# Optimization experiments

Measured on AMD Instinct MI355X. Metric: run time of the kernel, lower is better.

## Reference

```python
import jax, jax.numpy as jnp
import numpy as np

N = 4096
IN_DIM = 256
HID = 64
NHEADS = 4
OUT_DIM = 128
ALPHA = 0.5  # LeakyReLU negative slope
NEG_INF = -9e15


def gat_layer(x, mask, W, a, concat):
    """Dense GraphAttentionLayer (pyGAT style).
    x:[N,Fin], mask:[N,N] bool, W:[Fin,Fout], a:[2*Fout]."""
    Wh = x @ W                                   # [N, Fout]
    Fout = W.shape[1]
    f1 = Wh @ a[:Fout]                           # [N]
    f2 = Wh @ a[Fout:]                           # [N]
    e = jax.nn.leaky_relu(f1[:, None] + f2[None, :], negative_slope=ALPHA)  # [N,N]
    att = jax.nn.softmax(jnp.where(mask, e, NEG_INF), axis=1)               # [N,N]
    h = att @ Wh                                 # [N, Fout]
    return jax.nn.elu(h) if concat else h


def setup_inputs() -> dict:
    key = jax.random.key(0)
    ks = jax.random.split(key, 6)
    x = jax.random.normal(ks[0], (N, IN_DIM), dtype=jnp.float32)
    adj = jax.random.randint(ks[1], (N, N), 0, 2, dtype=jnp.int32)
    s_in = 1.0 / np.sqrt(IN_DIM)
    s_hid = 1.0 / np.sqrt(HID * NHEADS)
    W_heads = jax.random.uniform(ks[2], (NHEADS, IN_DIM, HID), jnp.float32, -s_in, s_in)
    a_heads = jax.random.uniform(ks[3], (NHEADS, 2 * HID), jnp.float32, -s_in, s_in)
    W_out = jax.random.uniform(ks[4], (HID * NHEADS, OUT_DIM), jnp.float32, -s_hid, s_hid)
    a_out = jax.random.uniform(ks[5], (2 * OUT_DIM,), jnp.float32, -s_hid, s_hid)
    return {"x": x, "adj": adj, "W_heads": W_heads, "a_heads": a_heads,
            "W_out": W_out, "a_out": a_out}


def reference(x, adj, W_heads, a_heads, W_out, a_out):
    mask = adj > 0
    # multi-head attention, concat along feature dim
    heads = jax.vmap(lambda W, a: gat_layer(x, mask, W, a, True))(W_heads, a_heads)
    h = jnp.transpose(heads, (1, 0, 2)).reshape(N, NHEADS * HID)  # [N, H*HID]
    # dropout=0 -> identity; final GAT layer (concat=False) + outer ELU
    out = jax.nn.elu(gat_layer(h, mask, W_out, a_out, False))     # [N, OUT_DIM]
    return out
```

## Files before the change

### kernel.cpp

```cpp
#include <hip/hip_runtime.h>
#include <hip/hip_bf16.h>

#define N 4096
#define IN_DIM 256
#define HID 64
#define NHEADS 4
#define OUT_DIM 128
#define LOG2E 1.44269504088896340736f

typedef __attribute__((ext_vector_type(8))) short bf16x8;
typedef __attribute__((ext_vector_type(4))) float f32x4;

__device__ __forceinline__ ushort2 bsplit(float v) {
    const ushort h = __hip_bfloat16_raw(__float2bfloat16(v)).x;
    const float vh = __uint_as_float((unsigned)h << 16);
    const ushort l = __hip_bfloat16_raw(__float2bfloat16(v - vh)).x;
    return make_ushort2(h, l);
}

__global__ __launch_bounds__(256, 4) void prep_kernel(
        const float* __restrict__ x, const float* __restrict__ W,
        const float* __restrict__ a, const int* __restrict__ adj,
        __hip_bfloat16* __restrict__ WhB,
        float* __restrict__ f1, float* __restrict__ f2,
        unsigned* __restrict__ maskT) {
    const int t = threadIdx.x;
    if (blockIdx.x < 256) {
        const int h = t >> 6, lane = t & 63, m = lane & 15, quad = lane >> 4;
        const int i0 = blockIdx.x * 16;
        const float* xrow = x + (size_t)(i0 + m) * IN_DIM;
        const float* Wp = W + (size_t)h * IN_DIM * HID;
        const f32x4 zero = {0.f, 0.f, 0.f, 0.f};
        f32x4 acc[4] = {zero, zero, zero, zero};
        for (int ks = 0; ks < 8; ks++) {
            const int kb = ks * 32 + quad * 8;
            const float4 xa = *(const float4*)(xrow + kb);
            const float4 xb = *(const float4*)(xrow + kb + 4);
            const float xf[8] = {xa.x, xa.y, xa.z, xa.w, xb.x, xb.y, xb.z, xb.w};
            bf16x8 xh, xl;
#pragma unroll
            for (int e = 0; e < 8; e++) {
                const ushort2 s = bsplit(xf[e]);
                xh[e] = (short)s.x; xl[e] = (short)s.y;
            }
#pragma unroll
            for (int ct = 0; ct < 4; ct++) {
                bf16x8 wh, wl;
#pragma unroll
                for (int e = 0; e < 8; e++) {
                    const ushort2 s =
                        bsplit(Wp[(size_t)(kb + e) * HID + ct * 16 + m]);
                    wh[e] = (short)s.x; wl[e] = (short)s.y;
                }
                acc[ct] = __builtin_amdgcn_mfma_f32_16x16x32_bf16(
                    xh, wh, acc[ct], 0, 0, 0);
                acc[ct] = __builtin_amdgcn_mfma_f32_16x16x32_bf16(
                    xl, wh, acc[ct], 0, 0, 0);
                acc[ct] = __builtin_amdgcn_mfma_f32_16x16x32_bf16(
                    xh, wl, acc[ct], 0, 0, 0);
            }
        }
        const int jblk = i0 >> 5, jb2 = (i0 >> 4) & 1;
#pragma unroll
        for (int ct = 0; ct < 4; ct++) {
#pragma unroll
            for (int r = 0; r < 4; r++) {
                const int jo = quad * 4 + r;
                const int lane_idx = m + 16 * (2 * jb2 + (jo >> 3));
                WhB[((((size_t)h * (N / 32) + jblk) * 4 + ct) * 64 + lane_idx) *
                        8 + (jo & 7)] = __float2bfloat16(acc[ct][r]);
            }
        }
        float av1[4], av2[4];
#pragma unroll
        for (int ct = 0; ct < 4; ct++) {
            av1[ct] = a[h * 2 * HID + ct * 16 + m];
            av2[ct] = a[h * 2 * HID + HID + ct * 16 + m];
        }
        float s1[4], s2[4];
#pragma unroll
        for (int r = 0; r < 4; r++) {
            s1[r] = 0.f; s2[r] = 0.f;
#pragma unroll
            for (int ct = 0; ct < 4; ct++) {
                s1[r] += acc[ct][r] * av1[ct];
                s2[r] += acc[ct][r] * av2[ct];
            }
        }
#pragma unroll
        for (int mm = 8; mm > 0; mm >>= 1) {
#pragma unroll
            for (int r = 0; r < 4; r++) {
                s1[r] += __shfl_xor(s1[r], mm, 64);
                s2[r] += __shfl_xor(s2[r], mm, 64);
            }
        }
        if (m == 0) {
#pragma unroll
            for (int r = 0; r < 4; r++) {
                f1[(size_t)h * N + i0 + quad * 4 + r] = s1[r] * LOG2E;
                f2[(size_t)h * N + i0 + quad * 4 + r] = s2[r] * LOG2E;
            }
        }
    } else {
        const int lane = t & 63, w = t >> 6;
        const int i = (blockIdx.x - 256) * 4 + w;
        const int4* arow = (const int4*)(adj + (size_t)i * N);
        for (int jb = 0; jb < N / 256; jb++) {
            const int4 a4 = arow[jb * 64 + lane];
            unsigned long long bal[4];
            bal[0] = __ballot(a4.x > 0);
            bal[1] = __ballot(a4.y > 0);
            bal[2] = __ballot(a4.z > 0);
            bal[3] = __ballot(a4.w > 0);
            if (lane < 8) {
                unsigned word = 0;
#pragma unroll
                for (int e = 0; e < 4; e++) {
                    unsigned xv = (unsigned)(bal[e] >> (8 * lane)) & 0xFFu;
                    xv = (xv | (xv << 12)) & 0x000F000Fu;
                    xv = (xv | (xv << 6))  & 0x03030303u;
                    xv = (xv | (xv << 3))  & 0x11111111u;
                    word |= xv << e;
                }
                maskT[(size_t)(jb * 8 + lane) * N + i] = word;
            }
        }
    }
}

template <int HEADS, int D, int DSL, int G, int MW>
__global__ __launch_bounds__(G * 64, 4) void attn_fused(
        const unsigned* __restrict__ maskT,
        const __hip_bfloat16* __restrict__ WhB,
        const float* __restrict__ f1g, const float* __restrict__ f2g,
        float* __restrict__ outp) {
    constexpr int CTtot = D / 16;
    constexpr int CTT = CTtot / DSL;
    constexpr int CC = (D == 64) ? 1 : 2;
    constexpr int KSTEPS = N / (32 * G);
    __shared__ float sh[MW * G * 16 * CC * 17];
    __shared__ float dsh[MW * G * 16];
    const int t = threadIdx.x;
    const int g = t >> 6, lane = t & 63;
    const int m = lane & 15, quad = lane >> 4;
    const int h = blockIdx.y / DSL, slc = blockIdx.y % DSL;
    const int i0 = blockIdx.x * (16 * MW);

    float f1v[MW];
#pragma unroll
    for (int mw = 0; mw < MW; mw++)
        f1v[mw] = f1g[(size_t)h * N + i0 + mw * 16 + m];
    const float* f2p = f2g + (size_t)h * N;
    const bf16x8* whb = (const bf16x8*)WhB + (size_t)h * (N / 32) * CTtot * 64;

    const f32x4 zero = {0.f, 0.f, 0.f, 0.f};
    f32x4 acc[MW][CTT];
    f32x4 sac[MW];
#pragma unroll
    for (int mw = 0; mw < MW; mw++) {
        sac[mw] = zero;
#pragma unroll
        for (int ct = 0; ct < CTT; ct++) acc[mw][ct] = zero;
    }
    const short one_bf = (short)0x3F80;
    const bf16x8 ones = {one_bf, one_bf, one_bf, one_bf,
                         one_bf, one_bf, one_bf, one_bf};

    unsigned mwrd[2][MW];
    float f2v[2][8];
    auto stage_mf = [&](int ks, int b) {
        const int j0 = g * (N / G) + ks * 32;
        const int jw = j0 >> 5;
#pragma unroll
        for (int mw = 0; mw < MW; mw++)
            mwrd[b][mw] = maskT[(size_t)jw * N + i0 + mw * 16 + m];
        const float4 lo = *(const float4*)(f2p + j0 + quad * 8);
        const float4 hi = *(const float4*)(f2p + j0 + quad * 8 + 4);
        f2v[b][0] = lo.x; f2v[b][1] = lo.y; f2v[b][2] = lo.z; f2v[b][3] = lo.w;
        f2v[b][4] = hi.x; f2v[b][5] = hi.y; f2v[b][6] = hi.z; f2v[b][7] = hi.w;
    };

    stage_mf(0, 0);
#pragma unroll 2
    for (int ks = 0; ks < KSTEPS; ks++) {
        const int cur = ks & 1;
        const int jwc = (g * (N / G) + ks * 32) >> 5;
        const bf16x8* bp = whb + ((size_t)jwc * CTtot + slc * CTT) * 64 + lane;
        bf16x8 bfrag[CTT];
#pragma unroll
        for (int ct = 0; ct < CTT; ct++) bfrag[ct] = bp[ct * 64];
        if (ks + 1 < KSTEPS) stage_mf(ks + 1, cur ^ 1);
        bf16x8 afr[MW];
#pragma unroll
        for (int mw = 0; mw < MW; mw++) {
            const unsigned mword = mwrd[cur][mw] >> (quad * 8);
            float p[8];
#pragma unroll
            for (int e = 0; e < 8; e++) {
                const float tt = f1v[mw] + f2v[cur][e];
                const float lr = fmaxf(tt, 0.5f * tt);
                const float pe = __builtin_amdgcn_exp2f(lr);
                p[e] = ((mword >> e) & 1u) ? pe : 0.f;
            }
            union { bf16x8 v; __hip_bfloat162 h2[4]; } u;
#pragma unroll
            for (int e2 = 0; e2 < 4; e2++)
                u.h2[e2] = __float22bfloat162_rn(
                    make_float2(p[2 * e2], p[2 * e2 + 1]));
            afr[mw] = u.v;
        }
#pragma unroll
        for (int ct = 0; ct < CTT; ct++)
#pragma unroll
            for (int mw = 0; mw < MW; mw++)
                acc[mw][ct] = __builtin_amdgcn_mfma_f32_16x16x32_bf16(
                    afr[mw], bfrag[ct], acc[mw][ct], 0, 0, 0);
#pragma unroll
        for (int mw = 0; mw < MW; mw++)
            sac[mw] = __builtin_amdgcn_mfma_f32_16x16x32_bf16(
                afr[mw], ones, sac[mw], 0, 0, 0);
    }

#pragma unroll
    for (int rd = 0; rd < CTT / CC; rd++) {
#pragma unroll
        for (int mw = 0; mw < MW; mw++) {
#pragma unroll
            for (int cc = 0; cc < CC; cc++) {
#pragma unroll
                for (int r = 0; r < 4; r++)
                    sh[(((mw * G + g) * 16 + quad * 4 + r) * CC + cc) * 17 + m] =
                        acc[mw][rd * CC + cc][r];
            }
            if (rd == 0 && m == 0) {
#pragma unroll
                for (int r = 0; r < 4; r++)
                    dsh[(mw * G + g) * 16 + quad * 4 + r] = sac[mw][r];
            }
        }
        __syncthreads();
        if (t < 16 * CC * 16) {
            int row, chl;
            if (D == 64) { row = t & 15; chl = (t >> 4) & 15; }
            else         { chl = t & 31; row = (t >> 5) & 15; }
#pragma unroll
            for (int mw = 0; mw < MW; mw++) {
                float av = 0.f, ss = 0.f;
#pragma unroll
                for (int gg = 0; gg < G; gg++) {
                    av += sh[(((mw * G + gg) * 16 + row) * CC + (chl >> 4)) * 17 +
                             (chl & 15)];
                    ss += dsh[(mw * G + gg) * 16 + row];
                }
                float v = av / ss;
                v = (v > 0.f) ? v : (__builtin_amdgcn_exp2f(v * LOG2E) - 1.f);
                const int chg = h * D + slc * (CTT * 16) + rd * CC * 16 + chl;
                const int irow = i0 + mw * 16 + row;
                if (D == 64)
                    outp[(size_t)irow * (NHEADS * HID) + chg] = v;
                else
                    outp[(size_t)irow * D + chg] = v;
            }
        }
        __syncthreads();
    }
}

__global__ __launch_bounds__(512, 2) void gemm2_kernel(
        const float* __restrict__ h1, const float* __restrict__ W2,
        const float* __restrict__ a2, __hip_bfloat16* __restrict__ WhB2,
        float* __restrict__ f1, float* __restrict__ f2) {
    __shared__ float fred[8][16][2];
    const int t = threadIdx.x;
    const int w = t >> 6, lane = t & 63, m = lane & 15, quad = lane >> 4;
    const int i0 = blockIdx.x * 16;
    const float* arow = h1 + (size_t)(i0 + m) * IN_DIM;
    const float* wp = W2 + w * 16 + m;
    const f32x4 zero = {0.f, 0.f, 0.f, 0.f};
    f32x4 acc = zero;
    for (int ks = 0; ks < 8; ks++) {
        const int kb = ks * 32 + quad * 8;
        const float4 xa = *(const float4*)(arow + kb);
        const float4 xb = *(const float4*)(arow + kb + 4);
        const float xf[8] = {xa.x, xa.y, xa.z, xa.w, xb.x, xb.y, xb.z, xb.w};
        bf16x8 xh, xl, wh, wl;
#pragma unroll
        for (int e = 0; e < 8; e++) {
            const ushort2 s = bsplit(xf[e]);
            xh[e] = (short)s.x; xl[e] = (short)s.y;
        }
#pragma unroll
        for (int e = 0; e < 8; e++) {
            const ushort2 s = bsplit(wp[(size_t)(kb + e) * OUT_DIM]);
            wh[e] = (short)s.x; wl[e] = (short)s.y;
        }
        acc = __builtin_amdgcn_mfma_f32_16x16x32_bf16(xh, wh, acc, 0, 0, 0);
        acc = __builtin_amdgcn_mfma_f32_16x16x32_bf16(xl, wh, acc, 0, 0, 0);
        acc = __builtin_amdgcn_mfma_f32_16x16x32_bf16(xh, wl, acc, 0, 0, 0);
    }
    const int jblk = i0 >> 5, jb2 = (i0 >> 4) & 1;
#pragma unroll
    for (int r = 0; r < 4; r++) {
        const int jo = quad * 4 + r;
        const int lane_idx = m + 16 * (2 * jb2 + (jo >> 3));
        WhB2[(((size_t)jblk * 8 + w) * 64 + lane_idx) * 8 + (jo & 7)] =
            __float2bfloat16(acc[r]);
    }
    const float av1 = a2[w * 16 + m], av2 = a2[OUT_DIM + w * 16 + m];
    float s1[4], s2[4];
#pragma unroll
    for (int r = 0; r < 4; r++) { s1[r] = acc[r] * av1; s2[r] = acc[r] * av2; }
#pragma unroll
    for (int mm = 8; mm > 0; mm >>= 1) {
#pragma unroll
        for (int r = 0; r < 4; r++) {
            s1[r] += __shfl_xor(s1[r], mm, 64);
            s2[r] += __shfl_xor(s2[r], mm, 64);
        }
    }
    if (m == 0) {
#pragma unroll
        for (int r = 0; r < 4; r++) {
            fred[w][quad * 4 + r][0] = s1[r];
            fred[w][quad * 4 + r][1] = s2[r];
        }
    }
    __syncthreads();
    if (t < 32) {
        const int row = t & 15, fn = t >> 4;
        float s = 0.f;
#pragma unroll
        for (int w8 = 0; w8 < 8; w8++) s += fred[w8][row][fn];
        (fn ? f2 : f1)[i0 + row] = s * LOG2E;
    }
}

extern "C" void kernel_launch(void* const* d_in, const int* in_sizes, int n_in,
                              void* d_out, int out_size, void* d_ws, size_t ws_size,
                              hipStream_t stream) {
    const float* x   = (const float*)d_in[0];
    const int*   adj = (const int*)d_in[1];
    const float* Wh_ = (const float*)d_in[2];
    const float* ah  = (const float*)d_in[3];
    const float* W2  = (const float*)d_in[4];
    const float* a2  = (const float*)d_in[5];
    float* out = (float*)d_out;

    float* ws = (float*)d_ws;
    float* f1a = ws;
    float* f2a = f1a + (size_t)NHEADS * N;
    float* f1b = f2a + (size_t)NHEADS * N;
    float* f2b = f1b + N;
    float* h1  = f2b + N;
    __hip_bfloat16* WhB1 = (__hip_bfloat16*)(h1 + (size_t)IN_DIM * N);
    __hip_bfloat16* WhB2 = WhB1 + (size_t)NHEADS * HID * N;
    unsigned* maskT = (unsigned*)(WhB2 + (size_t)OUT_DIM * N);

    prep_kernel<<<1280, 256, 0, stream>>>(x, Wh_, ah, adj, WhB1, f1a, f2a, maskT);
    attn_fused<NHEADS, HID, 1, 8, 2>
        <<<dim3(N / 32, NHEADS), 512, 0, stream>>>(maskT, WhB1, f1a, f2a, h1);
    gemm2_kernel<<<N / 16, 512, 0, stream>>>(h1, W2, a2, WhB2, f1b, f2b);
    attn_fused<1, OUT_DIM, 2, 8, 1>
        <<<dim3(N / 16, 2), 512, 0, stream>>>(maskT, WhB2, f1b, f2b, out);
}
```

Before: 169.2 us.

## Streamline attention inner loop and drop output-dim split in second layer

Replaces per-iteration index recomputation with incrementing pointers for the mask, f2 and Wh fragments. Masking moves from per-element selects to packed integer AND masks on the bf16 pairs. The second attention layer no longer splits the 128-wide output across two blocks, so each block computes all columns and the exp/softmax work is not duplicated. Launch bounds drop to 2 waves-per-SIMD occupancy so the larger accumulator set fits in registers, at the cost of less latency hiding and half as many blocks for layer 2.

```diff
diff --git a/kernel.cpp b/kernel.cpp
--- a/kernel.cpp
+++ b/kernel.cpp
@@ -130,7 +130,7 @@
 }
 
 template <int HEADS, int D, int DSL, int G, int MW>
-__global__ __launch_bounds__(G * 64, 4) void attn_fused(
+__global__ __launch_bounds__(G * 64, 2) void attn_fused(
         const unsigned* __restrict__ maskT,
         const __hip_bfloat16* __restrict__ WhB,
         const float* __restrict__ f1g, const float* __restrict__ f2g,
@@ -151,8 +151,12 @@
 #pragma unroll
     for (int mw = 0; mw < MW; mw++)
         f1v[mw] = f1g[(size_t)h * N + i0 + mw * 16 + m];
-    const float* f2p = f2g + (size_t)h * N;
-    const bf16x8* whb = (const bf16x8*)WhB + (size_t)h * (N / 32) * CTtot * 64;
+
+    const unsigned* mp = maskT + (size_t)(g * KSTEPS) * N + i0 + m;
+    const float* fp = f2g + (size_t)h * N + g * (N / G) + quad * 8;
+    const bf16x8* bp = (const bf16x8*)WhB +
+                       ((size_t)h * (N / 32) * CTtot +
+                        (size_t)(g * KSTEPS) * CTtot + slc * CTT) * 64 + lane;
 
     const f32x4 zero = {0.f, 0.f, 0.f, 0.f};
     f32x4 acc[MW][CTT];
@@ -168,46 +172,46 @@
                          one_bf, one_bf, one_bf, one_bf};
 
     unsigned mwrd[2][MW];
-    float f2v[2][8];
-    auto stage_mf = [&](int ks, int b) {
-        const int j0 = g * (N / G) + ks * 32;
-        const int jw = j0 >> 5;
-#pragma unroll
-        for (int mw = 0; mw < MW; mw++)
-            mwrd[b][mw] = maskT[(size_t)jw * N + i0 + mw * 16 + m];
-        const float4 lo = *(const float4*)(f2p + j0 + quad * 8);
-        const float4 hi = *(const float4*)(f2p + j0 + quad * 8 + 4);
-        f2v[b][0] = lo.x; f2v[b][1] = lo.y; f2v[b][2] = lo.z; f2v[b][3] = lo.w;
-        f2v[b][4] = hi.x; f2v[b][5] = hi.y; f2v[b][6] = hi.z; f2v[b][7] = hi.w;
+    float4 f2lo[2], f2hi[2];
+    auto stage = [&](int b) {
+#pragma unroll
+        for (int mw = 0; mw < MW; mw++) mwrd[b][mw] = mp[mw * 16];
+        f2lo[b] = *(const float4*)(fp);
+        f2hi[b] = *(const float4*)(fp + 4);
     };
 
-    stage_mf(0, 0);
+    stage(0); mp += N; fp += 32;
 #pragma unroll 2
     for (int ks = 0; ks < KSTEPS; ks++) {
         const int cur = ks & 1;
-        const int jwc = (g * (N / G) + ks * 32) >> 5;
-        const bf16x8* bp = whb + ((size_t)jwc * CTtot + slc * CTT) * 64 + lane;
         bf16x8 bfrag[CTT];
 #pragma unroll
         for (int ct = 0; ct < CTT; ct++) bfrag[ct] = bp[ct * 64];
-        if (ks + 1 < KSTEPS) stage_mf(ks + 1, cur ^ 1);
+        bp += CTtot * 64;
+        if (ks + 1 < KSTEPS) { stage(cur ^ 1); mp += N; fp += 32; }
+        const float fe[8] = {f2lo[cur].x, f2lo[cur].y, f2lo[cur].z, f2lo[cur].w,
+                             f2hi[cur].x, f2hi[cur].y, f2hi[cur].z, f2hi[cur].w};
         bf16x8 afr[MW];
 #pragma unroll
         for (int mw = 0; mw < MW; mw++) {
-            const unsigned mword = mwrd[cur][mw] >> (quad * 8);
+            const unsigned mword = (mwrd[cur][mw] >> (quad * 8)) & 0xFFu;
+            const unsigned spread = mword * 0x8001u;
             float p[8];
 #pragma unroll
             for (int e = 0; e < 8; e++) {
-                const float tt = f1v[mw] + f2v[cur][e];
+                const float tt = f1v[mw] + fe[e];
                 const float lr = fmaxf(tt, 0.5f * tt);
-                const float pe = __builtin_amdgcn_exp2f(lr);
-                p[e] = ((mword >> e) & 1u) ? pe : 0.f;
-            }
-            union { bf16x8 v; __hip_bfloat162 h2[4]; } u;
-#pragma unroll
-            for (int e2 = 0; e2 < 4; e2++)
+                p[e] = __builtin_amdgcn_exp2f(lr);
+            }
+            union { bf16x8 v; unsigned u32[4]; __hip_bfloat162 h2[4]; } u;
+#pragma unroll
+            for (int e2 = 0; e2 < 4; e2++) {
                 u.h2[e2] = __float22bfloat162_rn(
                     make_float2(p[2 * e2], p[2 * e2 + 1]));
+                const unsigned mk =
+                    ((spread >> (2 * e2)) & 0x00010001u) * 0xFFFFu;
+                u.u32[e2] &= mk;
+            }
             afr[mw] = u.v;
         }
 #pragma unroll
@@ -361,6 +365,6 @@
     attn_fused<NHEADS, HID, 1, 8, 2>
         <<<dim3(N / 32, NHEADS), 512, 0, stream>>>(maskT, WhB1, f1a, f2a, h1);
     gemm2_kernel<<<N / 16, 512, 0, stream>>>(h1, W2, a2, WhB2, f1b, f2b);
-    attn_fused<1, OUT_DIM, 2, 8, 1>
-        <<<dim3(N / 16, 2), 512, 0, stream>>>(maskT, WhB2, f1b, f2b, out);
-}
+    attn_fused<1, OUT_DIM, 1, 8, 1>
+        <<<dim3(N / 16, 1), 512, 0, stream>>>(maskT, WhB2, f1b, f2b, out);
+}
```

Result: no change. 166.1 us (-1.8%).
